# Kernel optimization log

Hardware: AMD Instinct MI355X
Metric: run time of the kernel (lower is better)

Reference implementation:

```python
import math
import jax, jax.numpy as jnp
from jax import lax
import numpy as np

# --- module hyperparameters (from init_kwargs) ---
NUM_POINTS = 4096
INIT_DIM = 64
STAGES = 4
K = 32
SIGMA = 0.26
BASELINE = 0.1
SCALING = 10.0
EPS = 1e-06
FEAT_NORMALIZE = True
IN_DIM = 3


def setup_inputs() -> dict:
    key = jax.random.key(0)
    xyz = jax.random.normal(key, (8, NUM_POINTS, 3), dtype=jnp.float32)
    return {"xyz": xyz}


def _adaptive_embed(x, out_dim):
    """Parameterless adaptive RBF/cosine embedding. x: [..., IN_DIM]."""
    if out_dim == 0:
        return x
    feat_dim = math.ceil(out_dim / IN_DIM)
    feat_val = jnp.asarray(np.linspace(-1.0, 1.0, feat_dim + 2)[1:-1], dtype=x.dtype)
    out_idx = np.linspace(0, feat_dim * IN_DIM - 1, out_dim).astype(np.int64)
    if x.ndim == 3:
        gstd = jnp.mean(jnp.std(x, axis=1, ddof=1))
    else:  # 4D [B, S, K, IN_DIM] -> std over flattened point axis
        B = x.shape[0]
        gstd = jnp.mean(jnp.std(x.reshape(B, -1, IN_DIM), axis=1, ddof=1))
    asig = SIGMA * (1.0 + gstd)
    blend = jax.nn.sigmoid((gstd - BASELINE) * SCALING)
    # tmp: [..., IN_DIM, feat_dim]; fused rbf/cos blend
    z = (x[..., None] - feat_val) / (asig + EPS)
    comb = blend * jnp.exp(-0.5 * z * z) + (1.0 - blend) * jnp.cos(z)
    pe = comb.reshape(*x.shape[:-1], IN_DIM * feat_dim)
    return pe[..., out_idx]


def _square_distance(src, dst):
    # [B,N,M] = |src|^2 + |dst|^2 - 2 src.dst
    d = -2.0 * jnp.einsum('bnc,bmc->bnm', src, dst)
    d += jnp.sum(src * src, -1)[:, :, None]
    d += jnp.sum(dst * dst, -1)[:, None, :]
    return d


def _fps(xyz, m):
    """Furthest point sampling (pointnet2 semantics: start at index 0). -> [B, m] int32"""
    B, N, _ = xyz.shape
    init_idx = jnp.zeros((B,), jnp.int32)
    dist0 = jnp.full((B, N), 1e10, dtype=xyz.dtype)

    def step(carry, _):
        dist, last = carry
        last_pt = jnp.take_along_axis(xyz, last[:, None, None].astype(jnp.int32), axis=1)  # [B,1,3]
        d = jnp.sum((xyz - last_pt) ** 2, -1)
        dist = jnp.minimum(dist, d)
        nxt = jnp.argmax(dist, axis=-1).astype(jnp.int32)
        return (dist, nxt), nxt

    (_, _), rest = lax.scan(step, (dist0, init_idx), None, length=m - 1)
    return jnp.concatenate([init_idx[None, :], rest], axis=0).T  # [B, m]


def _gather2(points, idx):
    # points [B,N,C], idx [B,S] -> [B,S,C]
    return jnp.take_along_axis(points, idx[..., None], axis=1)


def _gather3(points, idx):
    # points [B,N,C], idx [B,S,K] -> [B,S,K,C]
    B = points.shape[0]
    return points[jnp.arange(B)[:, None, None], idx]


def _normalize(center, knn, with_center):
    if with_center:
        diff = knn - center[:, :, None, :]
        std = jnp.clip(jnp.std(diff, axis=(0, 1, 3), keepdims=True, ddof=1), 1e-05, None)
        return diff / std
    std = jnp.clip(jnp.std(knn, axis=(0, 1), keepdims=True, ddof=1), 1e-05, None)
    return knn / std


def _forward(xyz):
    feat = _adaptive_embed(xyz, INIT_DIM)  # [B,N,INIT_DIM]
    x = xyz
    out_dim = INIT_DIM if INIT_DIM != 0 else 3
    stage_points = NUM_POINTS
    results = []
    for _ in range(STAGES):
        out_dim *= 2
        stage_points //= 2
        fps_idx = _fps(x, stage_points)                 # [B,S]
        xs = _gather2(x, fps_idx)                       # [B,S,3]
        fs = _gather2(feat, fps_idx)                    # [B,S,C]
        sqd = _square_distance(xs, x)                   # [B,S,N]
        _, knn_idx = lax.top_k(-sqd, K)                 # smallest distances
        xk = _gather3(x, knn_idx)                       # [B,S,K,3]
        fk = _gather3(feat, knn_idx)                    # [B,S,K,C]
        xk = _normalize(xs, xk, True)
        fk = _normalize(fs, fk, FEAT_NORMALIZE)
        fk = jnp.concatenate([fk, jnp.broadcast_to(fs[:, :, None, :], fk.shape)], axis=-1)  # [B,S,K,2C]
        pe = _adaptive_embed(xk, out_dim)               # [B,S,K,2C]
        fw = (fk + pe) * pe
        feat = jax.nn.gelu(fw.mean(-2) + fw.max(-2), approximate=False)  # [B,S,2C]
        x = xs
        results.append(jnp.concatenate([feat.max(1), feat.mean(1)], axis=1))  # [B, 4C]
    return jnp.concatenate(results, axis=1)


def reference(xyz):
    return _forward(xyz)
```

## Files before the change

kernel.cpp:

```cpp
#include <hip/hip_runtime.h>

typedef unsigned int u32;
typedef unsigned long long u64;
typedef float f32x2 __attribute__((ext_vector_type(2)));

#define WS_FEAT_A   0
#define WS_FEAT_B   8388608
#define WS_XS0      16777216
#define WS_XS1      16973824
#define WS_XS2      17072128
#define WS_XS3      17121280
#define WS_FP0      17145856
#define WS_FP1      17211392
#define WS_FP2      17244160
#define WS_FP3      17260544
#define WS_ACC      17268736
#define WS_ACCI     17281536
#define WS_PSTD     17281920
#define WS_PINIT    17282432
#define WS_KNN      17282560
#define WS_PMAX     19379712
#define WS_PSUM     19641856

__device__ __forceinline__ f32x2 pk_add(f32x2 a, f32x2 b) {
  f32x2 d;
  asm("v_pk_add_f32 %0, %1, %2" : "=v"(d) : "v"(a), "v"(b));
  return d;
}
__device__ __forceinline__ f32x2 pk_mul(f32x2 a, f32x2 b) {
  f32x2 d;
  asm("v_pk_mul_f32 %0, %1, %2" : "=v"(d) : "v"(a), "v"(b));
  return d;
}

__device__ __forceinline__ u32 dpp_umax_l63(u32 v) {
  u32 t;
  t = (u32)__builtin_amdgcn_update_dpp(0, (int)v, 0x111, 0xf, 0xf, true); v = t > v ? t : v;
  t = (u32)__builtin_amdgcn_update_dpp(0, (int)v, 0x112, 0xf, 0xf, true); v = t > v ? t : v;
  t = (u32)__builtin_amdgcn_update_dpp(0, (int)v, 0x114, 0xf, 0xf, true); v = t > v ? t : v;
  t = (u32)__builtin_amdgcn_update_dpp(0, (int)v, 0x118, 0xf, 0xf, true); v = t > v ? t : v;
  t = (u32)__builtin_amdgcn_update_dpp(0, (int)v, 0x142, 0xf, 0xf, true); v = t > v ? t : v;
  t = (u32)__builtin_amdgcn_update_dpp(0, (int)v, 0x143, 0xf, 0xf, true); v = t > v ? t : v;
  return (u32)__builtin_amdgcn_readlane((int)v, 63);
}

__device__ __forceinline__ u32 dpp_umin_l63(u32 v) {
  u32 t;
  t = (u32)__builtin_amdgcn_update_dpp(-1, (int)v, 0x111, 0xf, 0xf, false); v = t < v ? t : v;
  t = (u32)__builtin_amdgcn_update_dpp(-1, (int)v, 0x112, 0xf, 0xf, false); v = t < v ? t : v;
  t = (u32)__builtin_amdgcn_update_dpp(-1, (int)v, 0x114, 0xf, 0xf, false); v = t < v ? t : v;
  t = (u32)__builtin_amdgcn_update_dpp(-1, (int)v, 0x118, 0xf, 0xf, false); v = t < v ? t : v;
  t = (u32)__builtin_amdgcn_update_dpp(-1, (int)v, 0x142, 0xf, 0xf, false); v = t < v ? t : v;
  t = (u32)__builtin_amdgcn_update_dpp(-1, (int)v, 0x143, 0xf, 0xf, false); v = t < v ? t : v;
  return (u32)__builtin_amdgcn_readlane((int)v, 63);
}

__device__ __forceinline__ float sumsq3_nc(float x, float y, float z) {
#pragma clang fp contract(off)
  float d = x * x;
  d = d + y * y;
  d = d + z * z;
  return d;
}

__device__ __forceinline__ float knn_dist_nc(float qx, float qy, float qz, float qsq,
                                             float nx, float ny, float nz) {
#pragma clang fp contract(off)
  float dot = qx * nx;
  dot = dot + qy * ny;
  dot = dot + qz * nz;
  float nsq = nx * nx;
  nsq = nsq + ny * ny;
  nsq = nsq + nz * nz;
  float d = -2.0f * dot;
  d = d + qsq;
  d = d + nsq;
  return d;
}

template <int BLK, int P>
__device__ __forceinline__ void fps_body(const float* __restrict__ x,
                                         int* __restrict__ out_idx,
                                         float* __restrict__ xs, int S, int b) {
  constexpr int NW = BLK / 64;
  constexpr int PH = P / 2;
  const int N = BLK * P;
  const float* xb = x + (size_t)b * N * 3;
  const int tid = threadIdx.x;
  const int lane = tid & 63;
  const int wid = tid >> 6;

  __shared__ float4 spts[BLK * P];
  __shared__ alignas(16) u64 skey[2][NW < 2 ? 2 : NW];
  __shared__ int sidx[(NW > 1) ? (BLK * P / 2) : 1];

  f32x2 px2[PH], py2[PH], pz2[PH];
  float dist[P];
#pragma unroll
  for (int i = 0; i < P; ++i) {
    int idx = i * BLK + tid;
    float a = xb[idx * 3 + 0];
    float c = xb[idx * 3 + 1];
    float d = xb[idx * 3 + 2];
    px2[i >> 1][i & 1] = a;
    py2[i >> 1][i & 1] = c;
    pz2[i >> 1][i & 1] = d;
    dist[i] = 1e10f;
    spts[idx] = make_float4(a, c, d, 0.0f);
  }
  __syncthreads();

  float4 l4 = spts[0];
  float lx = l4.x, ly = l4.y, lz = l4.z;
  if constexpr (NW == 1) {
    if (tid == 0) {
      out_idx[b * S + 0] = 0;
      xs[(size_t)(b * S) * 3 + 0] = lx;
      xs[(size_t)(b * S) * 3 + 1] = ly;
      xs[(size_t)(b * S) * 3 + 2] = lz;
    }
  }

#pragma unroll 1
  for (int it = 1; it < S; ++it) {
    const int p = it & 1;
    f32x2 vnx, vny, vnz;
    vnx[0] = vnx[1] = __uint_as_float(__float_as_uint(lx) ^ 0x80000000u);
    vny[0] = vny[1] = __uint_as_float(__float_as_uint(ly) ^ 0x80000000u);
    vnz[0] = vnz[1] = __uint_as_float(__float_as_uint(lz) ^ 0x80000000u);
    u32 bd = 0;
    int bi = 0;
#pragma unroll
    for (int j = 0; j < PH; ++j) {
      f32x2 dx = pk_add(px2[j], vnx);
      f32x2 dy = pk_add(py2[j], vny);
      f32x2 dz = pk_add(pz2[j], vnz);
      f32x2 m0 = pk_mul(dx, dx);
      f32x2 m1 = pk_mul(dy, dy);
      f32x2 m2 = pk_mul(dz, dz);
      f32x2 s = pk_add(pk_add(m0, m1), m2);
#pragma unroll
      for (int h = 0; h < 2; ++h) {
        int i = 2 * j + h;
        float dm = fminf(dist[i], s[h]);
        dist[i] = dm;
        u32 db = __float_as_uint(dm);
        bool g = db > bd;
        bd = g ? db : bd;
        bi = g ? i : bi;
      }
    }
    u32 bidx = (u32)(bi * BLK + tid);

    u32 maxb = dpp_umax_l63(bd);
    u64 cm = __ballot(bd == maxb);
    u32 widx;
    if (__popcll(cm) == 1) {
      widx = (u32)__builtin_amdgcn_readlane((int)bidx, (int)__ffsll((long long)cm) - 1);
    } else {
      widx = 0xFFFFFFFFu - dpp_umax_l63((bd == maxb) ? (0xFFFFFFFFu - bidx) : 0u);
    }

    if constexpr (NW > 1) {
      if (lane == 0) skey[p][wid] = ((u64)maxb << 32) | (u64)(0xFFFFFFFFu - widx);
      __syncthreads();
      u64 best = skey[p][0];
#pragma unroll
      for (int w = 1; w < NW; ++w) {
        u64 kk = skey[p][w];
        best = (kk > best) ? kk : best;
      }
      widx = 0xFFFFFFFFu - (u32)best;
      if (tid == 0) sidx[it] = (int)widx;
    }

    float4 c4 = spts[widx];
    lx = c4.x;
    ly = c4.y;
    lz = c4.z;

    if constexpr (NW == 1) {
      if (lane == 0) {
        out_idx[b * S + it] = (int)widx;
        xs[(size_t)(b * S + it) * 3 + 0] = lx;
        xs[(size_t)(b * S + it) * 3 + 1] = ly;
        xs[(size_t)(b * S + it) * 3 + 2] = lz;
      }
    }
  }

  if constexpr (NW > 1) {
    __syncthreads();
    for (int i = tid; i < S; i += BLK) {
      int idx = (i == 0) ? 0 : sidx[i];
      out_idx[b * S + i] = idx;
      float4 c4 = spts[idx];
      xs[(size_t)(b * S + i) * 3 + 0] = c4.x;
      xs[(size_t)(b * S + i) * 3 + 1] = c4.y;
      xs[(size_t)(b * S + i) * 3 + 2] = c4.z;
    }
  }
}

template <int BLK, int P>
__global__ __launch_bounds__(BLK) void fps_kernel(const float* __restrict__ x,
                                                  int* __restrict__ out_idx,
                                                  float* __restrict__ xs, int S) {
  fps_body<BLK, P>(x, out_idx, xs, S, blockIdx.x);
}

template <int P>
__device__ __forceinline__ void knn_body(const float* __restrict__ x,
                                         const float* __restrict__ xs,
                                         int* __restrict__ knn, int S, int q, int lane) {
  int b = q / S;
  const int N = 64 * P;
  const float* xb = x + (size_t)b * N * 3;
  float qx = xs[(size_t)q * 3 + 0];
  float qy = xs[(size_t)q * 3 + 1];
  float qz = xs[(size_t)q * 3 + 2];
  float qsq = sumsq3_nc(qx, qy, qz);

  u64 key[P];
#pragma unroll
  for (int i = 0; i < P; ++i) {
    int idx = i * 64 + lane;
    float nx = xb[idx * 3 + 0], ny = xb[idx * 3 + 1], nz = xb[idx * 3 + 2];
    float d = knn_dist_nc(qx, qy, qz, qsq, nx, ny, nz);
    u32 u = __float_as_uint(d);
    u32 msk = ((u32)(((int)u) >> 31)) | 0x80000000u;
    u ^= msk;
    key[i] = ((u64)u << 32) | (u64)(u32)idx;
  }

  u64 prev = 0;
  u32 myv = 0;
#pragma unroll 1
  for (int r = 0; r < 32; ++r) {
    u64 best = ~0ull;
#pragma unroll
    for (int i = 0; i < P; ++i) {
      u64 k = key[i];
      u64 cand = (k > prev) ? k : ~0ull;
      best = (cand < best) ? cand : best;
    }
    u32 hi = (u32)(best >> 32);
    u32 minb = dpp_umin_l63(hi);
    u64 cm = __ballot(hi == minb);
    u32 lo;
    if (__popcll(cm) == 1) {
      lo = (u32)__builtin_amdgcn_readlane((int)(u32)best, (int)__ffsll((long long)cm) - 1);
    } else {
      lo = dpp_umin_l63(hi == minb ? (u32)best : 0xFFFFFFFFu);
    }
    prev = ((u64)minb << 32) | lo;
    if (lane == r) myv = lo;
  }
  if (lane < 32) knn[(size_t)q * 32 + lane] = (int)myv;
}

template <int P>
__global__ __launch_bounds__(256) void knn_kernel(const float* __restrict__ x,
                                                  const float* __restrict__ xs,
                                                  int* __restrict__ knn, int S) {
  knn_body<P>(x, xs, knn, S, blockIdx.x * 4 + (threadIdx.x >> 6), threadIdx.x & 63);
}

template <int FBLK, int FP, int KP, int KWPB>
__global__ __launch_bounds__(FBLK) void co_fps_knn(const float* __restrict__ xf,
                                                   int* __restrict__ fps_out,
                                                   float* __restrict__ xs_out, int Sn,
                                                   const float* __restrict__ xk,
                                                   const float* __restrict__ xsq,
                                                   int* __restrict__ knn_out, int Sk) {
  if (blockIdx.x < 8) {
    fps_body<FBLK, FP>(xf, fps_out, xs_out, Sn, blockIdx.x);
  } else {
    int lane = threadIdx.x & 63;
    int q = (blockIdx.x - 8) * KWPB + (KWPB > 1 ? (int)(threadIdx.x >> 6) : 0);
    knn_body<KP>(xk, xsq, knn_out, Sk, q, lane);
  }
}

template <int C>
__global__ __launch_bounds__(256) void stats1_kernel(const float* __restrict__ x,
                                                     const float* __restrict__ xs,
                                                     const float* __restrict__ feat,
                                                     const int* __restrict__ fidx,
                                                     const int* __restrict__ knn,
                                                     double* __restrict__ acc, int S, int N) {
  int k = threadIdx.x & 31;
  int qs = threadIdx.x >> 5;
  int qbase = blockIdx.x * 32;
  int b = qbase / S;
  double sx[3] = {0, 0, 0}, sxx[3] = {0, 0, 0}, sf = 0, sff = 0;
  for (int jj = 0; jj < 4; ++jj) {
    int q = qbase + qs * 4 + jj;
    int nbr = knn[(size_t)q * 32 + k];
    int fq = fidx[q];
    const float* xr = x + ((size_t)b * N + nbr) * 3;
    const float* xq = xs + (size_t)q * 3;
#pragma unroll
    for (int c = 0; c < 3; ++c) {
      float d = xr[c] - xq[c];
      sx[c] += (double)d;
      sxx[c] += (double)d * (double)d;
    }
    const float4* fr = (const float4*)(feat + ((size_t)b * N + nbr) * C);
    const float4* fqv = (const float4*)(feat + ((size_t)b * N + fq) * C);
    for (int c = 0; c < C / 4; ++c) {
      float4 a = fr[c], bb = fqv[c];
      float d0 = a.x - bb.x, d1 = a.y - bb.y, d2 = a.z - bb.z, d3 = a.w - bb.w;
      sf += (double)d0 + (double)d1 + (double)d2 + (double)d3;
      sff += (double)d0 * d0 + (double)d1 * d1 + (double)d2 * d2 + (double)d3 * d3;
    }
  }
  __shared__ double red[256];
  double vals[8] = {sx[0], sxx[0], sx[1], sxx[1], sx[2], sxx[2], sf, sff};
  double* accG = acc;
  double* acc_fk = acc + 1536;
#pragma unroll
  for (int p = 0; p < 8; ++p) {
    red[threadIdx.x] = vals[p];
    __syncthreads();
    if (threadIdx.x < 32) {
      double r = 0;
#pragma unroll
      for (int t = 0; t < 8; ++t) r += red[k + t * 32];
      if (p < 6) {
        int c = p >> 1;
        atomicAdd(&accG[((b * 3 + c) * 32 + k) * 2 + (p & 1)], r);
      } else {
        atomicAdd(&acc_fk[k * 2 + (p & 1)], r);
      }
    }
    __syncthreads();
  }
}

__global__ void fin_kernel(double* __restrict__ acc, float* __restrict__ pstd, int S, int C) {
  __shared__ float sisx[32];
  __shared__ double gslot[24];
  int tid = threadIdx.x;
  const double* accG = acc;
  const double* afk = acc + 1536;
  if (tid < 32) {
    double sd = 0, sdd = 0;
    for (int bc = 0; bc < 24; ++bc) {
      sd += accG[(bc * 32 + tid) * 2];
      sdd += accG[(bc * 32 + tid) * 2 + 1];
    }
    int n1 = 8 * S * 3;
    double var = (sdd - sd * sd / (double)n1) / (double)(n1 - 1);
    float st = fmaxf((float)sqrt(var > 0.0 ? var : 0.0), 1e-5f);
    sisx[tid] = 1.0f / st;
    pstd[tid] = sisx[tid];
    double s = afk[tid * 2], ss = afk[tid * 2 + 1];
    int n2 = 8 * S * C;
    var = (ss - s * s / (double)n2) / (double)(n2 - 1);
    st = fmaxf((float)sqrt(var > 0.0 ? var : 0.0), 1e-5f);
    pstd[32 + tid] = 1.0f / st;
  }
  __syncthreads();
  if (tid < 24) {
    double A = 0, B = 0;
    for (int k = 0; k < 32; ++k) {
      double is = (double)sisx[k];
      A += is * accG[(tid * 32 + k) * 2];
      B += is * is * accG[(tid * 32 + k) * 2 + 1];
    }
    int ng = S * 32;
    double var = (B - A * A / (double)ng) / (double)(ng - 1);
    gslot[tid] = sqrt(var > 0.0 ? var : 0.0);
  }
  __syncthreads();
  if (tid == 0) {
    double g = 0;
    for (int i = 0; i < 24; ++i) g += gslot[i];
    float gstd = (float)(g / 24.0);
    float asig = 0.26f * (1.0f + gstd);
    pstd[64] = 1.0f / (asig + 1e-6f);
    pstd[65] = 1.0f / (1.0f + expf(-(gstd - 0.1f) * 10.0f));
  }
  __syncthreads();
  for (int i = tid; i < 1600; i += 64) acc[i] = 0.0;
}

__global__ __launch_bounds__(256) void init_stats(const float* __restrict__ xyz,
                                                  double* __restrict__ acc) {
  int bc = blockIdx.x;
  int b = bc / 3, c = bc - b * 3;
  double s = 0, ss = 0;
  for (int n = threadIdx.x; n < 4096; n += 256) {
    float v = xyz[((size_t)b * 4096 + n) * 3 + c];
    s += (double)v;
    ss += (double)v * (double)v;
  }
  __shared__ double r1[256], r2[256];
  r1[threadIdx.x] = s;
  r2[threadIdx.x] = ss;
  __syncthreads();
  for (int off = 128; off > 0; off >>= 1) {
    if (threadIdx.x < off) {
      r1[threadIdx.x] += r1[threadIdx.x + off];
      r2[threadIdx.x] += r2[threadIdx.x + off];
    }
    __syncthreads();
  }
  if (threadIdx.x == 0) {
    acc[bc * 2] = r1[0];
    acc[bc * 2 + 1] = r2[0];
  }
}

__global__ void fin_init(const double* __restrict__ acc, float* __restrict__ params,
                         double* __restrict__ accz) {
  if (threadIdx.x == 0) {
    double g = 0;
    for (int i = 0; i < 24; ++i) {
      double s = acc[i * 2], ss = acc[i * 2 + 1];
      double var = (ss - s * s / 4096.0) / 4095.0;
      g += sqrt(var > 0.0 ? var : 0.0);
    }
    float gstd = (float)(g / 24.0);
    float asig = 0.26f * (1.0f + gstd);
    params[0] = 1.0f / (asig + 1e-6f);
    params[1] = 1.0f / (1.0f + expf(-(gstd - 0.1f) * 10.0f));
  }
  __syncthreads();
  for (int i = threadIdx.x; i < 1600; i += 64) accz[i] = 0.0;
}

__global__ __launch_bounds__(256) void init_embed(const float* __restrict__ xyz,
                                                  const float* __restrict__ params,
                                                  float* __restrict__ feat) {
  int t = blockIdx.x * 256 + threadIdx.x;
  int j = t & 63;
  int n = (t >> 6) & 4095;
  int b = t >> 18;
  float inv_ae = params[0], blend = params[1];
  int idx = (int)((double)j * 65.0 / 63.0);
  int c = idx / 22, f = idx - c * 22;
  float fv = (float)(-1.0 + 2.0 * (double)(f + 1) / 23.0);
  float v = xyz[((size_t)b * 4096 + n) * 3 + c];
  float z = (v - fv) * inv_ae;
  float e = __expf(-0.5f * z * z);
  float co = __cosf(z);
  feat[t] = blend * e + (1.0f - blend) * co;
}

template <int C, int TWOC, int BLK, int FD>
__global__ __launch_bounds__(BLK) void fused_kernel(const float* __restrict__ x,
                                                    const float* __restrict__ xs,
                                                    const float* __restrict__ feat_in,
                                                    const int* __restrict__ fidx,
                                                    const int* __restrict__ knn,
                                                    const float* __restrict__ pstd,
                                                    float* __restrict__ feat_out, int S, int N) {
  constexpr int JPT = TWOC / BLK;
  int q = blockIdx.x;
  int b = q / S;
  int tid = threadIdx.x;
  float inv_ae = pstd[64];
  float blend = pstd[65];
  float omb = 1.0f - blend;
  float c0 = xs[(size_t)q * 3 + 0];
  float c1 = xs[(size_t)q * 3 + 1];
  float c2 = xs[(size_t)q * 3 + 2];
  const float* fsrow = feat_in + ((size_t)b * N + fidx[q]) * C;

  int cj[JPT];
  float fvj[JPT], fj[JPT], sum[JPT], mx[JPT];
#pragma unroll
  for (int i = 0; i < JPT; ++i) {
    int j = tid + i * BLK;
    int idx = (int)((double)j * (double)(3 * FD - 1) / (double)(TWOC - 1));
    int c = idx / FD, f = idx - c * FD;
    cj[i] = c;
    fvj[i] = (float)(-1.0 + 2.0 * (double)(f + 1) / (double)(FD + 1));
    fj[i] = fsrow[j < C ? j : j - C];
    sum[i] = 0.0f;
    mx[i] = -3.4e38f;
  }

  const int* krow = knn + (size_t)q * 32;
#pragma unroll 1
  for (int k = 0; k < 32; ++k) {
    int nbr = krow[k];
    float isx = pstd[k], isf = pstd[32 + k];
    const float* xr = x + ((size_t)b * N + nbr) * 3;
    float xk0 = (xr[0] - c0) * isx;
    float xk1 = (xr[1] - c1) * isx;
    float xk2 = (xr[2] - c2) * isx;
    const float* fr = feat_in + ((size_t)b * N + nbr) * C;
#pragma unroll
    for (int i = 0; i < JPT; ++i) {
      int j = tid + i * BLK;
      float cat;
      if (j < C)
        cat = (fr[j] - fj[i]) * isf;
      else
        cat = fj[i];
      float xc = (cj[i] == 0) ? xk0 : ((cj[i] == 1) ? xk1 : xk2);
      float z = (xc - fvj[i]) * inv_ae;
      float comb = blend * __expf(-0.5f * z * z) + omb * __cosf(z);
      float fw = (cat + comb) * comb;
      sum[i] += fw;
      mx[i] = fmaxf(mx[i], fw);
    }
  }
#pragma unroll
  for (int i = 0; i < JPT; ++i) {
    float val = sum[i] * 0.03125f + mx[i];
    float g = 0.5f * val * (1.0f + erff(val * 0.7071067811865476f));
    feat_out[(size_t)q * TWOC + tid + i * BLK] = g;
  }
}

template <int TWOC, int BLK>
__global__ __launch_bounds__(BLK) void result_partial(const float* __restrict__ feat,
                                                      float* __restrict__ pmax,
                                                      double* __restrict__ psum, int S) {
  int j = blockIdx.x * BLK + threadIdx.x;
  int ch = blockIdx.y, b = blockIdx.z;
  int rows = S >> 3;
  int s0 = ch * rows;
  float m = -3.4e38f;
  double sd = 0.0;
  for (int s = 0; s < rows; ++s) {
    float v = feat[((size_t)(b * S + s0 + s)) * TWOC + j];
    m = fmaxf(m, v);
    sd += (double)v;
  }
  pmax[((size_t)ch * 8 + b) * TWOC + j] = m;
  psum[((size_t)ch * 8 + b) * TWOC + j] = sd;
}

__global__ void result_final(const float* __restrict__ pmax, const double* __restrict__ psum,
                             float* __restrict__ out, int TWOC, int off, int S) {
  int t = blockIdx.x * 256 + threadIdx.x;
  if (t >= 8 * TWOC) return;
  int b = t / TWOC, j = t - b * TWOC;
  float m = -3.4e38f;
  double sd = 0.0;
  for (int ch = 0; ch < 8; ++ch) {
    m = fmaxf(m, pmax[((size_t)ch * 8 + b) * TWOC + j]);
    sd += psum[((size_t)ch * 8 + b) * TWOC + j];
  }
  out[(size_t)b * 3840 + off + j] = m;
  out[(size_t)b * 3840 + off + TWOC + j] = (float)(sd / (double)S);
}

template <int N, int S, int C, int TWOC, int FD, int BLKF>
static void run_tail(const float* x, const float* xs, const float* feat_in, const int* fidx,
                     const int* knnb, double* acc, float* pstd, float* feat_out, float* pmax,
                     double* psum, float* out, int outoff, hipStream_t stream) {
  stats1_kernel<C><<<(8 * S) / 32, 256, 0, stream>>>(x, xs, feat_in, fidx, knnb, acc, S, N);
  fin_kernel<<<1, 64, 0, stream>>>(acc, pstd, S, C);
  fused_kernel<C, TWOC, BLKF, FD><<<8 * S, BLKF, 0, stream>>>(x, xs, feat_in, fidx, knnb, pstd,
                                                              feat_out, S, N);
  constexpr int RBLK = (TWOC < 256) ? TWOC : 256;
  result_partial<TWOC, RBLK><<<dim3(TWOC / RBLK, 8, 8), RBLK, 0, stream>>>(feat_out, pmax, psum, S);
  result_final<<<(8 * TWOC + 255) / 256, 256, 0, stream>>>(pmax, psum, out, TWOC, outoff, S);
}

extern "C" void kernel_launch(void* const* d_in, const int* in_sizes, int n_in, void* d_out,
                              int out_size, void* d_ws, size_t ws_size, hipStream_t stream) {
  (void)in_sizes;
  (void)n_in;
  (void)out_size;
  (void)ws_size;
  const float* xyz = (const float*)d_in[0];
  float* out = (float*)d_out;
  char* w = (char*)d_ws;

  float* featA = (float*)(w + WS_FEAT_A);
  float* featB = (float*)(w + WS_FEAT_B);
  float* xs0 = (float*)(w + WS_XS0);
  float* xs1 = (float*)(w + WS_XS1);
  float* xs2 = (float*)(w + WS_XS2);
  float* xs3 = (float*)(w + WS_XS3);
  int* fp0 = (int*)(w + WS_FP0);
  int* fp1 = (int*)(w + WS_FP1);
  int* fp2 = (int*)(w + WS_FP2);
  int* fp3 = (int*)(w + WS_FP3);
  int* knnb = (int*)(w + WS_KNN);
  float* pmax = (float*)(w + WS_PMAX);
  double* psum = (double*)(w + WS_PSUM);
  double* acc = (double*)(w + WS_ACC);
  double* acci = (double*)(w + WS_ACCI);
  float* pstd = (float*)(w + WS_PSTD);
  float* pinit = (float*)(w + WS_PINIT);

  init_stats<<<24, 256, 0, stream>>>(xyz, acci);
  fin_init<<<1, 64, 0, stream>>>(acci, pinit, acc);
  init_embed<<<(8 * 4096 * 64) / 256, 256, 0, stream>>>(xyz, pinit, featA);

  fps_kernel<256, 16><<<8, 256, 0, stream>>>(xyz, fp0, xs0, 2048);
  co_fps_knn<256, 8, 64, 4><<<8 + 4096, 256, 0, stream>>>(xs0, fp1, xs1, 1024,
                                                          xyz, xs0, knnb, 2048);
  run_tail<4096, 2048, 64, 128, 43, 128>(xyz, xs0, featA, fp0, knnb, acc, pstd, featB,
                                         pmax, psum, out, 0, stream);

  co_fps_knn<64, 16, 32, 1><<<8 + 8192, 64, 0, stream>>>(xs1, fp2, xs2, 512,
                                                         xs0, xs1, knnb, 1024);
  run_tail<2048, 1024, 128, 256, 86, 256>(xs0, xs1, featB, fp1, knnb, acc, pstd, featA,
                                          pmax, psum, out, 256, stream);

  co_fps_knn<64, 8, 16, 1><<<8 + 4096, 64, 0, stream>>>(xs2, fp3, xs3, 256,
                                                        xs1, xs2, knnb, 512);
  run_tail<1024, 512, 256, 512, 171, 256>(xs1, xs2, featA, fp2, knnb, acc, pstd, featB,
                                          pmax, psum, out, 768, stream);

  knn_kernel<8><<<512, 256, 0, stream>>>(xs2, xs3, knnb, 256);
  run_tail<512, 256, 512, 1024, 342, 256>(xs2, xs3, featB, fp3, knnb, acc, pstd, featA,
                                          pmax, psum, out, 1792, stream);
}
```

Measured before the change: 2.576 ms.

## Co-schedule FPS with embed, kNN, stats and fused stages across kernels

```diff
diff --git a/kernel.cpp b/kernel.cpp
--- a/kernel.cpp
+++ b/kernel.cpp
@@ -18,9 +18,12 @@
 #define WS_ACCI     17281536
 #define WS_PSTD     17281920
 #define WS_PINIT    17282432
-#define WS_KNN      17282560
-#define WS_PMAX     19379712
-#define WS_PSUM     19641856
+#define WS_KN0      17282560
+#define WS_KN1      19379712
+#define WS_KN2      20428288
+#define WS_KN3      20952576
+#define WS_PMAX     21214720
+#define WS_PSUM     21476864
 
 __device__ __forceinline__ f32x2 pk_add(f32x2 a, f32x2 b) {
   f32x2 d;
@@ -108,7 +111,11 @@
     dist[i] = 1e10f;
     spts[idx] = make_float4(a, c, d, 0.0f);
   }
-  __syncthreads();
+  if constexpr (NW > 1) {
+    __syncthreads();
+  } else {
+    asm volatile("s_waitcnt lgkmcnt(0)" ::: "memory");
+  }
 
   float4 l4 = spts[0];
   float lx = l4.x, ly = l4.y, lz = l4.z;
@@ -200,13 +207,6 @@
       xs[(size_t)(b * S + i) * 3 + 2] = c4.z;
     }
   }
-}
-
-template <int BLK, int P>
-__global__ __launch_bounds__(BLK) void fps_kernel(const float* __restrict__ x,
-                                                  int* __restrict__ out_idx,
-                                                  float* __restrict__ xs, int S) {
-  fps_body<BLK, P>(x, out_idx, xs, S, blockIdx.x);
 }
 
 template <int P>
@@ -259,39 +259,16 @@
   if (lane < 32) knn[(size_t)q * 32 + lane] = (int)myv;
 }
 
-template <int P>
-__global__ __launch_bounds__(256) void knn_kernel(const float* __restrict__ x,
-                                                  const float* __restrict__ xs,
-                                                  int* __restrict__ knn, int S) {
-  knn_body<P>(x, xs, knn, S, blockIdx.x * 4 + (threadIdx.x >> 6), threadIdx.x & 63);
-}
-
-template <int FBLK, int FP, int KP, int KWPB>
-__global__ __launch_bounds__(FBLK) void co_fps_knn(const float* __restrict__ xf,
-                                                   int* __restrict__ fps_out,
-                                                   float* __restrict__ xs_out, int Sn,
-                                                   const float* __restrict__ xk,
-                                                   const float* __restrict__ xsq,
-                                                   int* __restrict__ knn_out, int Sk) {
-  if (blockIdx.x < 8) {
-    fps_body<FBLK, FP>(xf, fps_out, xs_out, Sn, blockIdx.x);
-  } else {
-    int lane = threadIdx.x & 63;
-    int q = (blockIdx.x - 8) * KWPB + (KWPB > 1 ? (int)(threadIdx.x >> 6) : 0);
-    knn_body<KP>(xk, xsq, knn_out, Sk, q, lane);
-  }
-}
-
 template <int C>
-__global__ __launch_bounds__(256) void stats1_kernel(const float* __restrict__ x,
-                                                     const float* __restrict__ xs,
-                                                     const float* __restrict__ feat,
-                                                     const int* __restrict__ fidx,
-                                                     const int* __restrict__ knn,
-                                                     double* __restrict__ acc, int S, int N) {
+__device__ __forceinline__ void stats1_body(const float* __restrict__ x,
+                                            const float* __restrict__ xs,
+                                            const float* __restrict__ feat,
+                                            const int* __restrict__ fidx,
+                                            const int* __restrict__ knn,
+                                            double* __restrict__ acc, int S, int N, int bid) {
   int k = threadIdx.x & 31;
   int qs = threadIdx.x >> 5;
-  int qbase = blockIdx.x * 32;
+  int qbase = bid * 32;
   int b = qbase / S;
   double sx[3] = {0, 0, 0}, sxx[3] = {0, 0, 0}, sf = 0, sff = 0;
   for (int jj = 0; jj < 4; ++jj) {
@@ -338,127 +315,25 @@
   }
 }
 
-__global__ void fin_kernel(double* __restrict__ acc, float* __restrict__ pstd, int S, int C) {
-  __shared__ float sisx[32];
-  __shared__ double gslot[24];
-  int tid = threadIdx.x;
-  const double* accG = acc;
-  const double* afk = acc + 1536;
-  if (tid < 32) {
-    double sd = 0, sdd = 0;
-    for (int bc = 0; bc < 24; ++bc) {
-      sd += accG[(bc * 32 + tid) * 2];
-      sdd += accG[(bc * 32 + tid) * 2 + 1];
-    }
-    int n1 = 8 * S * 3;
-    double var = (sdd - sd * sd / (double)n1) / (double)(n1 - 1);
-    float st = fmaxf((float)sqrt(var > 0.0 ? var : 0.0), 1e-5f);
-    sisx[tid] = 1.0f / st;
-    pstd[tid] = sisx[tid];
-    double s = afk[tid * 2], ss = afk[tid * 2 + 1];
-    int n2 = 8 * S * C;
-    var = (ss - s * s / (double)n2) / (double)(n2 - 1);
-    st = fmaxf((float)sqrt(var > 0.0 ? var : 0.0), 1e-5f);
-    pstd[32 + tid] = 1.0f / st;
-  }
-  __syncthreads();
-  if (tid < 24) {
-    double A = 0, B = 0;
-    for (int k = 0; k < 32; ++k) {
-      double is = (double)sisx[k];
-      A += is * accG[(tid * 32 + k) * 2];
-      B += is * is * accG[(tid * 32 + k) * 2 + 1];
-    }
-    int ng = S * 32;
-    double var = (B - A * A / (double)ng) / (double)(ng - 1);
-    gslot[tid] = sqrt(var > 0.0 ? var : 0.0);
-  }
-  __syncthreads();
-  if (tid == 0) {
-    double g = 0;
-    for (int i = 0; i < 24; ++i) g += gslot[i];
-    float gstd = (float)(g / 24.0);
-    float asig = 0.26f * (1.0f + gstd);
-    pstd[64] = 1.0f / (asig + 1e-6f);
-    pstd[65] = 1.0f / (1.0f + expf(-(gstd - 0.1f) * 10.0f));
-  }
-  __syncthreads();
-  for (int i = tid; i < 1600; i += 64) acc[i] = 0.0;
-}
-
-__global__ __launch_bounds__(256) void init_stats(const float* __restrict__ xyz,
-                                                  double* __restrict__ acc) {
-  int bc = blockIdx.x;
-  int b = bc / 3, c = bc - b * 3;
-  double s = 0, ss = 0;
-  for (int n = threadIdx.x; n < 4096; n += 256) {
-    float v = xyz[((size_t)b * 4096 + n) * 3 + c];
-    s += (double)v;
-    ss += (double)v * (double)v;
-  }
-  __shared__ double r1[256], r2[256];
-  r1[threadIdx.x] = s;
-  r2[threadIdx.x] = ss;
-  __syncthreads();
-  for (int off = 128; off > 0; off >>= 1) {
-    if (threadIdx.x < off) {
-      r1[threadIdx.x] += r1[threadIdx.x + off];
-      r2[threadIdx.x] += r2[threadIdx.x + off];
-    }
-    __syncthreads();
-  }
-  if (threadIdx.x == 0) {
-    acc[bc * 2] = r1[0];
-    acc[bc * 2 + 1] = r2[0];
-  }
-}
-
-__global__ void fin_init(const double* __restrict__ acc, float* __restrict__ params,
-                         double* __restrict__ accz) {
-  if (threadIdx.x == 0) {
-    double g = 0;
-    for (int i = 0; i < 24; ++i) {
-      double s = acc[i * 2], ss = acc[i * 2 + 1];
-      double var = (ss - s * s / 4096.0) / 4095.0;
-      g += sqrt(var > 0.0 ? var : 0.0);
-    }
-    float gstd = (float)(g / 24.0);
-    float asig = 0.26f * (1.0f + gstd);
-    params[0] = 1.0f / (asig + 1e-6f);
-    params[1] = 1.0f / (1.0f + expf(-(gstd - 0.1f) * 10.0f));
-  }
-  __syncthreads();
-  for (int i = threadIdx.x; i < 1600; i += 64) accz[i] = 0.0;
-}
-
-__global__ __launch_bounds__(256) void init_embed(const float* __restrict__ xyz,
-                                                  const float* __restrict__ params,
-                                                  float* __restrict__ feat) {
-  int t = blockIdx.x * 256 + threadIdx.x;
-  int j = t & 63;
-  int n = (t >> 6) & 4095;
-  int b = t >> 18;
-  float inv_ae = params[0], blend = params[1];
-  int idx = (int)((double)j * 65.0 / 63.0);
-  int c = idx / 22, f = idx - c * 22;
-  float fv = (float)(-1.0 + 2.0 * (double)(f + 1) / 23.0);
-  float v = xyz[((size_t)b * 4096 + n) * 3 + c];
-  float z = (v - fv) * inv_ae;
-  float e = __expf(-0.5f * z * z);
-  float co = __cosf(z);
-  feat[t] = blend * e + (1.0f - blend) * co;
+template <int C>
+__global__ __launch_bounds__(256) void stats1_kernel(const float* __restrict__ x,
+                                                     const float* __restrict__ xs,
+                                                     const float* __restrict__ feat,
+                                                     const int* __restrict__ fidx,
+                                                     const int* __restrict__ knn,
+                                                     double* __restrict__ acc, int S, int N) {
+  stats1_body<C>(x, xs, feat, fidx, knn, acc, S, N, blockIdx.x);
 }
 
 template <int C, int TWOC, int BLK, int FD>
-__global__ __launch_bounds__(BLK) void fused_kernel(const float* __restrict__ x,
-                                                    const float* __restrict__ xs,
-                                                    const float* __restrict__ feat_in,
-                                                    const int* __restrict__ fidx,
-                                                    const int* __restrict__ knn,
-                                                    const float* __restrict__ pstd,
-                                                    float* __restrict__ feat_out, int S, int N) {
+__device__ __forceinline__ void fused_body(const float* __restrict__ x,
+                                           const float* __restrict__ xs,
+                                           const float* __restrict__ feat_in,
+                                           const int* __restrict__ fidx,
+                                           const int* __restrict__ knn,
+                                           const float* __restrict__ pstd,
+                                           float* __restrict__ feat_out, int S, int N, int q) {
   constexpr int JPT = TWOC / BLK;
-  int q = blockIdx.x;
   int b = q / S;
   int tid = threadIdx.x;
   float inv_ae = pstd[64];
@@ -514,6 +389,211 @@
     float val = sum[i] * 0.03125f + mx[i];
     float g = 0.5f * val * (1.0f + erff(val * 0.7071067811865476f));
     feat_out[(size_t)q * TWOC + tid + i * BLK] = g;
+  }
+}
+
+template <int C, int TWOC, int BLK, int FD>
+__global__ __launch_bounds__(BLK) void fused_kernel(const float* __restrict__ x,
+                                                    const float* __restrict__ xs,
+                                                    const float* __restrict__ feat_in,
+                                                    const int* __restrict__ fidx,
+                                                    const int* __restrict__ knn,
+                                                    const float* __restrict__ pstd,
+                                                    float* __restrict__ feat_out, int S, int N) {
+  fused_body<C, TWOC, BLK, FD>(x, xs, feat_in, fidx, knn, pstd, feat_out, S, N, blockIdx.x);
+}
+
+__global__ void fin_kernel(double* __restrict__ acc, float* __restrict__ pstd, int S, int C) {
+  __shared__ float sisx[32];
+  __shared__ double gslot[24];
+  int tid = threadIdx.x;
+  const double* accG = acc;
+  const double* afk = acc + 1536;
+  if (tid < 32) {
+    double sd = 0, sdd = 0;
+    for (int bc = 0; bc < 24; ++bc) {
+      sd += accG[(bc * 32 + tid) * 2];
+      sdd += accG[(bc * 32 + tid) * 2 + 1];
+    }
+    int n1 = 8 * S * 3;
+    double var = (sdd - sd * sd / (double)n1) / (double)(n1 - 1);
+    float st = fmaxf((float)sqrt(var > 0.0 ? var : 0.0), 1e-5f);
+    sisx[tid] = 1.0f / st;
+    pstd[tid] = sisx[tid];
+    double s = afk[tid * 2], ss = afk[tid * 2 + 1];
+    int n2 = 8 * S * C;
+    var = (ss - s * s / (double)n2) / (double)(n2 - 1);
+    st = fmaxf((float)sqrt(var > 0.0 ? var : 0.0), 1e-5f);
+    pstd[32 + tid] = 1.0f / st;
+  }
+  __syncthreads();
+  if (tid < 24) {
+    double A = 0, B = 0;
+    for (int k = 0; k < 32; ++k) {
+      double is = (double)sisx[k];
+      A += is * accG[(tid * 32 + k) * 2];
+      B += is * is * accG[(tid * 32 + k) * 2 + 1];
+    }
+    int ng = S * 32;
+    double var = (B - A * A / (double)ng) / (double)(ng - 1);
+    gslot[tid] = sqrt(var > 0.0 ? var : 0.0);
+  }
+  __syncthreads();
+  if (tid == 0) {
+    double g = 0;
+    for (int i = 0; i < 24; ++i) g += gslot[i];
+    float gstd = (float)(g / 24.0);
+    float asig = 0.26f * (1.0f + gstd);
+    pstd[64] = 1.0f / (asig + 1e-6f);
+    pstd[65] = 1.0f / (1.0f + expf(-(gstd - 0.1f) * 10.0f));
+  }
+  __syncthreads();
+  for (int i = tid; i < 1600; i += 64) acc[i] = 0.0;
+}
+
+__global__ __launch_bounds__(256) void init_stats(const float* __restrict__ xyz,
+                                                  double* __restrict__ acc) {
+  int bc = blockIdx.x;
+  int b = bc / 3, c = bc - b * 3;
+  double s = 0, ss = 0;
+  for (int n = threadIdx.x; n < 4096; n += 256) {
+    float v = xyz[((size_t)b * 4096 + n) * 3 + c];
+    s += (double)v;
+    ss += (double)v * (double)v;
+  }
+  __shared__ double r1[256], r2[256];
+  r1[threadIdx.x] = s;
+  r2[threadIdx.x] = ss;
+  __syncthreads();
+  for (int off = 128; off > 0; off >>= 1) {
+    if (threadIdx.x < off) {
+      r1[threadIdx.x] += r1[threadIdx.x + off];
+      r2[threadIdx.x] += r2[threadIdx.x + off];
+    }
+    __syncthreads();
+  }
+  if (threadIdx.x == 0) {
+    acc[bc * 2] = r1[0];
+    acc[bc * 2 + 1] = r2[0];
+  }
+}
+
+__global__ void fin_init(const double* __restrict__ acc, float* __restrict__ params,
+                         double* __restrict__ accz) {
+  if (threadIdx.x == 0) {
+    double g = 0;
+    for (int i = 0; i < 24; ++i) {
+      double s = acc[i * 2], ss = acc[i * 2 + 1];
+      double var = (ss - s * s / 4096.0) / 4095.0;
+      g += sqrt(var > 0.0 ? var : 0.0);
+    }
+    float gstd = (float)(g / 24.0);
+    float asig = 0.26f * (1.0f + gstd);
+    params[0] = 1.0f / (asig + 1e-6f);
+    params[1] = 1.0f / (1.0f + expf(-(gstd - 0.1f) * 10.0f));
+  }
+  __syncthreads();
+  for (int i = threadIdx.x; i < 1600; i += 64) accz[i] = 0.0;
+}
+
+__device__ __forceinline__ void init_embed_body(const float* __restrict__ xyz,
+                                                const float* __restrict__ params,
+                                                float* __restrict__ feat, int t) {
+  int j = t & 63;
+  int n = (t >> 6) & 4095;
+  int b = t >> 18;
+  float inv_ae = params[0], blend = params[1];
+  int idx = (int)((double)j * 65.0 / 63.0);
+  int c = idx / 22, f = idx - c * 22;
+  float fv = (float)(-1.0 + 2.0 * (double)(f + 1) / 23.0);
+  float v = xyz[((size_t)b * 4096 + n) * 3 + c];
+  float z = (v - fv) * inv_ae;
+  float e = __expf(-0.5f * z * z);
+  float co = __cosf(z);
+  feat[t] = blend * e + (1.0f - blend) * co;
+}
+
+__global__ __launch_bounds__(256) void co_a_kernel(const float* __restrict__ xyz,
+                                                   int* __restrict__ fp0,
+                                                   float* __restrict__ xs0,
+                                                   const float* __restrict__ pinit,
+                                                   float* __restrict__ featA) {
+  if (blockIdx.x < 8) {
+    fps_body<256, 16>(xyz, fp0, xs0, 2048, blockIdx.x);
+  } else {
+    init_embed_body(xyz, pinit, featA, (blockIdx.x - 8) * 256 + threadIdx.x);
+  }
+}
+
+__global__ __launch_bounds__(256) void co_b_kernel(const float* __restrict__ xs0,
+                                                   int* __restrict__ fp1,
+                                                   float* __restrict__ xs1,
+                                                   const float* __restrict__ xyz,
+                                                   int* __restrict__ kn0) {
+  if (blockIdx.x < 8) {
+    fps_body<256, 8>(xs0, fp1, xs1, 1024, blockIdx.x);
+  } else {
+    knn_body<64>(xyz, xs0, kn0, 2048, (blockIdx.x - 8) * 4 + (threadIdx.x >> 6),
+                 threadIdx.x & 63);
+  }
+}
+
+__global__ __launch_bounds__(256) void co_c_kernel(const float* __restrict__ xs1,
+                                                   int* __restrict__ fp2,
+                                                   float* __restrict__ xs2,
+                                                   const float* __restrict__ xs0,
+                                                   int* __restrict__ kn1,
+                                                   const float* __restrict__ xyz,
+                                                   const float* __restrict__ featA,
+                                                   const int* __restrict__ fp0,
+                                                   const int* __restrict__ kn0,
+                                                   double* __restrict__ acc) {
+  int bid = blockIdx.x;
+  if (bid < 8) {
+    if (threadIdx.x < 64) fps_body<64, 16>(xs1, fp2, xs2, 512, bid);
+  } else if (bid < 2056) {
+    knn_body<32>(xs0, xs1, kn1, 1024, (bid - 8) * 4 + (threadIdx.x >> 6), threadIdx.x & 63);
+  } else {
+    stats1_body<64>(xyz, xs0, featA, fp0, kn0, acc, 2048, 4096, bid - 2056);
+  }
+}
+
+__global__ __launch_bounds__(128) void co_d_kernel(const float* __restrict__ xs2,
+                                                   int* __restrict__ fp3,
+                                                   float* __restrict__ xs3,
+                                                   const float* __restrict__ xs1,
+                                                   int* __restrict__ kn2,
+                                                   const float* __restrict__ xyz,
+                                                   const float* __restrict__ xs0,
+                                                   const float* __restrict__ featA,
+                                                   const int* __restrict__ fp0,
+                                                   const int* __restrict__ kn0,
+                                                   const float* __restrict__ pstd,
+                                                   float* __restrict__ featB) {
+  int bid = blockIdx.x;
+  if (bid < 8) {
+    if (threadIdx.x < 64) fps_body<64, 8>(xs2, fp3, xs3, 256, bid);
+  } else if (bid < 2056) {
+    knn_body<16>(xs1, xs2, kn2, 512, (bid - 8) * 2 + (threadIdx.x >> 6), threadIdx.x & 63);
+  } else {
+    fused_body<64, 128, 128, 43>(xyz, xs0, featA, fp0, kn0, pstd, featB, 2048, 4096, bid - 2056);
+  }
+}
+
+__global__ __launch_bounds__(256) void co_e_kernel(const float* __restrict__ xs2,
+                                                   const float* __restrict__ xs3,
+                                                   int* __restrict__ kn3,
+                                                   const float* __restrict__ xs0,
+                                                   const float* __restrict__ xs1,
+                                                   const float* __restrict__ featB,
+                                                   const int* __restrict__ fp1,
+                                                   const int* __restrict__ kn1,
+                                                   double* __restrict__ acc) {
+  int bid = blockIdx.x;
+  if (bid < 512) {
+    knn_body<8>(xs2, xs3, kn3, 256, bid * 4 + (threadIdx.x >> 6), threadIdx.x & 63);
+  } else {
+    stats1_body<128>(xs0, xs1, featB, fp1, kn1, acc, 1024, 2048, bid - 512);
   }
 }
 
@@ -551,19 +631,6 @@
   out[(size_t)b * 3840 + off + TWOC + j] = (float)(sd / (double)S);
 }
 
-template <int N, int S, int C, int TWOC, int FD, int BLKF>
-static void run_tail(const float* x, const float* xs, const float* feat_in, const int* fidx,
-                     const int* knnb, double* acc, float* pstd, float* feat_out, float* pmax,
-                     double* psum, float* out, int outoff, hipStream_t stream) {
-  stats1_kernel<C><<<(8 * S) / 32, 256, 0, stream>>>(x, xs, feat_in, fidx, knnb, acc, S, N);
-  fin_kernel<<<1, 64, 0, stream>>>(acc, pstd, S, C);
-  fused_kernel<C, TWOC, BLKF, FD><<<8 * S, BLKF, 0, stream>>>(x, xs, feat_in, fidx, knnb, pstd,
-                                                              feat_out, S, N);
-  constexpr int RBLK = (TWOC < 256) ? TWOC : 256;
-  result_partial<TWOC, RBLK><<<dim3(TWOC / RBLK, 8, 8), RBLK, 0, stream>>>(feat_out, pmax, psum, S);
-  result_final<<<(8 * TWOC + 255) / 256, 256, 0, stream>>>(pmax, psum, out, TWOC, outoff, S);
-}
-
 extern "C" void kernel_launch(void* const* d_in, const int* in_sizes, int n_in, void* d_out,
                               int out_size, void* d_ws, size_t ws_size, hipStream_t stream) {
   (void)in_sizes;
@@ -584,7 +651,10 @@
   int* fp1 = (int*)(w + WS_FP1);
   int* fp2 = (int*)(w + WS_FP2);
   int* fp3 = (int*)(w + WS_FP3);
-  int* knnb = (int*)(w + WS_KNN);
+  int* kn0 = (int*)(w + WS_KN0);
+  int* kn1 = (int*)(w + WS_KN1);
+  int* kn2 = (int*)(w + WS_KN2);
+  int* kn3 = (int*)(w + WS_KN3);
   float* pmax = (float*)(w + WS_PMAX);
   double* psum = (double*)(w + WS_PSUM);
   double* acc = (double*)(w + WS_ACC);
@@ -594,25 +664,36 @@
 
   init_stats<<<24, 256, 0, stream>>>(xyz, acci);
   fin_init<<<1, 64, 0, stream>>>(acci, pinit, acc);
-  init_embed<<<(8 * 4096 * 64) / 256, 256, 0, stream>>>(xyz, pinit, featA);
-
-  fps_kernel<256, 16><<<8, 256, 0, stream>>>(xyz, fp0, xs0, 2048);
-  co_fps_knn<256, 8, 64, 4><<<8 + 4096, 256, 0, stream>>>(xs0, fp1, xs1, 1024,
-                                                          xyz, xs0, knnb, 2048);
-  run_tail<4096, 2048, 64, 128, 43, 128>(xyz, xs0, featA, fp0, knnb, acc, pstd, featB,
-                                         pmax, psum, out, 0, stream);
-
-  co_fps_knn<64, 16, 32, 1><<<8 + 8192, 64, 0, stream>>>(xs1, fp2, xs2, 512,
-                                                         xs0, xs1, knnb, 1024);
-  run_tail<2048, 1024, 128, 256, 86, 256>(xs0, xs1, featB, fp1, knnb, acc, pstd, featA,
-                                          pmax, psum, out, 256, stream);
-
-  co_fps_knn<64, 8, 16, 1><<<8 + 4096, 64, 0, stream>>>(xs2, fp3, xs3, 256,
-                                                        xs1, xs2, knnb, 512);
-  run_tail<1024, 512, 256, 512, 171, 256>(xs1, xs2, featA, fp2, knnb, acc, pstd, featB,
-                                          pmax, psum, out, 768, stream);
-
-  knn_kernel<8><<<512, 256, 0, stream>>>(xs2, xs3, knnb, 256);
-  run_tail<512, 256, 512, 1024, 342, 256>(xs2, xs3, featB, fp3, knnb, acc, pstd, featA,
-                                          pmax, psum, out, 1792, stream);
-}
+  co_a_kernel<<<8 + 8192, 256, 0, stream>>>(xyz, fp0, xs0, pinit, featA);
+
+  co_b_kernel<<<8 + 4096, 256, 0, stream>>>(xs0, fp1, xs1, xyz, kn0);
+
+  co_c_kernel<<<2568, 256, 0, stream>>>(xs1, fp2, xs2, xs0, kn1, xyz, featA, fp0, kn0, acc);
+  fin_kernel<<<1, 64, 0, stream>>>(acc, pstd, 2048, 64);
+
+  co_d_kernel<<<2056 + 16384, 128, 0, stream>>>(xs2, fp3, xs3, xs1, kn2, xyz, xs0, featA, fp0,
+                                                kn0, pstd, featB);
+  result_partial<128, 128><<<dim3(1, 8, 8), 128, 0, stream>>>(featB, pmax, psum, 2048);
+  result_final<<<(8 * 128 + 255) / 256, 256, 0, stream>>>(pmax, psum, out, 128, 0, 2048);
+
+  co_e_kernel<<<768, 256, 0, stream>>>(xs2, xs3, kn3, xs0, xs1, featB, fp1, kn1, acc);
+  fin_kernel<<<1, 64, 0, stream>>>(acc, pstd, 1024, 128);
+  fused_kernel<128, 256, 256, 86><<<8192, 256, 0, stream>>>(xs0, xs1, featB, fp1, kn1, pstd,
+                                                            featA, 1024, 2048);
+  result_partial<256, 256><<<dim3(1, 8, 8), 256, 0, stream>>>(featA, pmax, psum, 1024);
+  result_final<<<(8 * 256 + 255) / 256, 256, 0, stream>>>(pmax, psum, out, 256, 256, 1024);
+
+  stats1_kernel<256><<<128, 256, 0, stream>>>(xs1, xs2, featA, fp2, kn2, acc, 512, 1024);
+  fin_kernel<<<1, 64, 0, stream>>>(acc, pstd, 512, 256);
+  fused_kernel<256, 512, 256, 171><<<4096, 256, 0, stream>>>(xs1, xs2, featA, fp2, kn2, pstd,
+                                                             featB, 512, 1024);
+  result_partial<512, 256><<<dim3(2, 8, 8), 256, 0, stream>>>(featB, pmax, psum, 512);
+  result_final<<<(8 * 512 + 255) / 256, 256, 0, stream>>>(pmax, psum, out, 512, 768, 512);
+
+  stats1_kernel<512><<<64, 256, 0, stream>>>(xs2, xs3, featB, fp3, kn3, acc, 256, 512);
+  fin_kernel<<<1, 64, 0, stream>>>(acc, pstd, 256, 512);
+  fused_kernel<512, 1024, 256, 342><<<2048, 256, 0, stream>>>(xs2, xs3, featB, fp3, kn3, pstd,
+                                                              featA, 256, 512);
+  result_partial<1024, 256><<<dim3(4, 8, 8), 256, 0, stream>>>(featA, pmax, psum, 256);
+  result_final<<<(8 * 1024 + 255) / 256, 256, 0, stream>>>(pmax, psum, out, 1024, 1792, 256);
+}
```

New measurement: 2.472 ms. 1.04x faster.
